# Optimization experiments

Measured on AMD Instinct MI355X. Metric: run time of the kernel, lower is better.

The kernel has to match this reference:

```python
import jax, jax.numpy as jnp
import numpy as np

WINDOW = 3
SEQ_LEN = 41
FEATURE = 128
FILTER_NUM = 128
PAD = WINDOW // 2


def setup_inputs() -> dict:
    key = jax.random.key(0)
    k1, k2 = jax.random.split(key)
    B = 4096
    inputs = jax.random.normal(k1, (B, SEQ_LEN, FEATURE), dtype=jnp.float32)
    # per-position Linear weights: 41 independent [window*feature -> filter_num] layers
    fan_in = WINDOW * FEATURE
    W = jax.random.normal(k2, (SEQ_LEN, fan_in, FILTER_NUM), dtype=jnp.float32) / np.sqrt(fan_in)
    b = jnp.zeros((SEQ_LEN, FILTER_NUM), dtype=jnp.float32)
    return {"inputs": inputs, "W": W, "b": b}


def reference(inputs, W, b):
    # inputs: [B, S, F]; pad sequence dim by PAD zeros on each side
    xpad = jnp.pad(inputs, ((0, 0), (PAD, PAD), (0, 0)))  # [B, S+2*PAD, F]
    # gather windows: idx[s, w] = s + w -> [B, S, WINDOW, F]
    idx = jnp.arange(SEQ_LEN)[:, None] + jnp.arange(WINDOW)[None, :]
    xw = xpad[:, idx, :]
    B = inputs.shape[0]
    xw = xw.reshape(B, SEQ_LEN, WINDOW * FEATURE)  # [B, S, W*F]
    # per-position linear (locally-connected): one batched GEMM over positions
    out = jnp.einsum('bsd,sdf->bsf', xw, W) + b[None, :, :]
    # ReLU; Dropout(0.5) is identity in eval mode
    return jax.nn.relu(out)
```

## Files before the change

kernel.cpp:

```cpp
#include <hip/hip_runtime.h>

#define SEQ 41
#define FEAT 128
#define KDIM 384
#define ROWLEN (SEQ * FEAT)
#define BM 128

typedef float floatx4 __attribute__((ext_vector_type(4)));
typedef __bf16 bf16x8 __attribute__((ext_vector_type(8)));
typedef unsigned short ushortx4 __attribute__((ext_vector_type(4)));
typedef unsigned short ushortx8 __attribute__((ext_vector_type(8)));

__device__ __forceinline__ unsigned short f2bf(float f) {
    unsigned int u = __builtin_bit_cast(unsigned int, f);
    return (unsigned short)((u + 0x7fffu + ((u >> 16) & 1u)) >> 16);
}

#define DMA16(g, l)                                                          \
    __builtin_amdgcn_global_load_lds(                                        \
        (const __attribute__((address_space(1))) void*)(g),                  \
        (__attribute__((address_space(3))) void*)(l), 16, 0, 0)

__global__ __launch_bounds__(256) void wt2_kernel(const float* __restrict__ W,
                                                  unsigned short* __restrict__ Wt2) {
    int t = blockIdx.x * 256 + threadIdx.x;
    int s = t / 6144, g = t % 6144;
    int lane = g & 63, nt = (g >> 6) & 7, ks = (g >> 9) & 1, slab = g >> 10;
    int n  = nt * 16 + (lane & 15);
    int k0 = slab * 64 + ks * 32 + (lane >> 4) * 8;
    const float* Ws = W + (size_t)s * KDIM * FEAT;
    ushortx8 v;
#pragma unroll
    for (int j = 0; j < 8; j++) v[j] = f2bf(Ws[(size_t)(k0 + j) * FEAT + n]);
    *reinterpret_cast<ushortx8*>(Wt2 + (size_t)t * 8) = v;
}

template <int USE_WT>
__global__ __launch_bounds__(256, 2) void gemm_kernel(const float* __restrict__ X,
                                                      const void* __restrict__ Wsrc,
                                                      const float* __restrict__ bias,
                                                      float* __restrict__ out) {
    __shared__ unsigned short Afrag[2][2][8][512];
    __shared__ unsigned short Bfrag[2][2][8][512];

    const int tid  = threadIdx.x;
    const int lane = tid & 63;
    const int wv   = tid >> 6;
    const int s    = blockIdx.y;
    const int m0   = blockIdx.x * BM;

    const int klo = (s == 0) ? 2 : 0;
    const int khi = (s == SEQ - 1) ? 4 : 6;
    const int nk  = khi - klo;
    const int obase = (s - 1) * FEAT;

    const int colq = lane & 15, quad = lane >> 4;
    const int wr = wv >> 1, wc = wv & 1;

    const int ar = tid >> 3;
    const int ag = tid & 7;
    const int aq = ag >> 1, ahalf = ag & 1;

    const unsigned short* Wt2 = (const unsigned short*)Wsrc;
    const float* Wf = (const float*)Wsrc;

    floatx4 acc[4][4];
#pragma unroll
    for (int i = 0; i < 4; i++)
#pragma unroll
        for (int j = 0; j < 4; j++) acc[i][j] = (floatx4){0.f, 0.f, 0.f, 0.f};

    floatx4 a0[4], a1[4];

    auto stageA_load = [&](int kki) {
#pragma unroll
        for (int p = 0; p < 4; p++) {
            const float* base = X + (size_t)(m0 + p * 32 + ar) * ROWLEN
                                  + obase + kki * 64 + ag * 4;
            a0[p] = *reinterpret_cast<const floatx4*>(base);
            a1[p] = *reinterpret_cast<const floatx4*>(base + 32);
        }
    };
    auto stageA_write = [&](int buf) {
#pragma unroll
        for (int p = 0; p < 4; p++) {
            int r  = p * 32 + ar;
            int mt = r >> 4;
            int sl = ((r & 15) + 16 * aq) * 8 + ahalf * 4;
            ushortx4 w0, w1;
#pragma unroll
            for (int e = 0; e < 4; e++) { w0[e] = f2bf(a0[p][e]); w1[e] = f2bf(a1[p][e]); }
            *reinterpret_cast<ushortx4*>(&Afrag[buf][0][mt][sl]) = w0;
            *reinterpret_cast<ushortx4*>(&Afrag[buf][1][mt][sl]) = w1;
        }
    };
    auto stageB = [&](int buf, int kki) {
        if (USE_WT) {
            const unsigned short* src = Wt2 + (size_t)(s * 6 + kki) * 8192;
#pragma unroll
            for (int j = 0; j < 4; j++) {
                int fid = wv * 4 + j;
                const unsigned short* g = src + fid * 512 + lane * 8;
                DMA16(g, &Bfrag[buf][fid >> 3][fid & 7][0]);
            }
        } else {
#pragma unroll
            for (int p = 0; p < 4; p++) {
                int g2 = p * 256 + tid;
                int ln = g2 & 63, nt = (g2 >> 6) & 7, ks = (g2 >> 9) & 1;
                int n = nt * 16 + (ln & 15);
                int k = kki * 64 + ks * 32 + (ln >> 4) * 8;
                ushortx8 v;
#pragma unroll
                for (int j = 0; j < 8; j++)
                    v[j] = f2bf(Wf[((size_t)s * KDIM + k + j) * FEAT + n]);
                *reinterpret_cast<ushortx8*>(&Bfrag[buf][ks][nt][ln * 8]) = v;
            }
        }
    };
    auto compute = [&](int buf) {
#pragma unroll
        for (int ks = 0; ks < 2; ks++) {
            bf16x8 af[4], bf[4];
#pragma unroll
            for (int i = 0; i < 4; i++)
                af[i] = *reinterpret_cast<const bf16x8*>(&Afrag[buf][ks][wr * 4 + i][lane * 8]);
#pragma unroll
            for (int i = 0; i < 4; i++)
                bf[i] = *reinterpret_cast<const bf16x8*>(&Bfrag[buf][ks][wc * 4 + i][lane * 8]);
#pragma unroll
            for (int mi = 0; mi < 4; mi++)
#pragma unroll
                for (int ni = 0; ni < 4; ni++)
                    acc[mi][ni] = __builtin_amdgcn_mfma_f32_16x16x32_bf16(
                        af[mi], bf[ni], acc[mi][ni], 0, 0, 0);
        }
    };

    stageA_load(klo);
    stageB(0, klo);
    stageA_write(0);

    for (int i = 0; i < nk; i++) {
        __syncthreads();
        int cur = i & 1, nxt = cur ^ 1;
        if (i + 1 < nk) {
            stageA_load(klo + i + 1);
            stageB(nxt, klo + i + 1);
        }
        compute(cur);
        if (i + 1 < nk) stageA_write(nxt);
    }

#pragma unroll
    for (int mi = 0; mi < 4; mi++) {
        int m = m0 + (wr * 4 + mi) * 16 + quad * 4;
#pragma unroll
        for (int ni = 0; ni < 4; ni++) {
            int n = (wc * 4 + ni) * 16 + colq;
            float bv = bias[s * FEAT + n];
#pragma unroll
            for (int r = 0; r < 4; r++) {
                float v = acc[mi][ni][r] + bv;
                v = v > 0.f ? v : 0.f;
                out[((size_t)(m + r) * SEQ + s) * FEAT + n] = v;
            }
        }
    }
}

extern "C" void kernel_launch(void* const* d_in, const int* in_sizes, int n_in,
                              void* d_out, int out_size, void* d_ws, size_t ws_size,
                              hipStream_t stream) {
    const float* X    = (const float*)d_in[0];
    const float* W    = (const float*)d_in[1];
    const float* bias = (const float*)d_in[2];
    float* out = (float*)d_out;

    const int B = in_sizes[0] / ROWLEN;
    dim3 grid(B / BM, SEQ);

    const size_t wt_bytes = (size_t)SEQ * 6 * 8192 * sizeof(unsigned short);
    if (ws_size >= wt_bytes) {
        unsigned short* Wt2 = (unsigned short*)d_ws;
        wt2_kernel<<<(SEQ * 6144) / 256, 256, 0, stream>>>(W, Wt2);
        gemm_kernel<1><<<grid, 256, 0, stream>>>(X, (const void*)Wt2, bias, out);
    } else {
        gemm_kernel<0><<<grid, 256, 0, stream>>>(X, (const void*)W, bias, out);
    }
}
```

Before: 184.0 us.

## Drop LDS staging; load MFMA fragments directly from global per wave

```diff
diff --git a/kernel.cpp b/kernel.cpp
--- a/kernel.cpp
+++ b/kernel.cpp
@@ -8,7 +8,6 @@
 
 typedef float floatx4 __attribute__((ext_vector_type(4)));
 typedef __bf16 bf16x8 __attribute__((ext_vector_type(8)));
-typedef unsigned short ushortx4 __attribute__((ext_vector_type(4)));
 typedef unsigned short ushortx8 __attribute__((ext_vector_type(8)));
 
 __device__ __forceinline__ unsigned short f2bf(float f) {
@@ -16,10 +15,12 @@
     return (unsigned short)((u + 0x7fffu + ((u >> 16) & 1u)) >> 16);
 }
 
-#define DMA16(g, l)                                                          \
-    __builtin_amdgcn_global_load_lds(                                        \
-        (const __attribute__((address_space(1))) void*)(g),                  \
-        (__attribute__((address_space(3))) void*)(l), 16, 0, 0)
+__device__ __forceinline__ bf16x8 pack8(floatx4 lo, floatx4 hi) {
+    bf16x8 r;
+#pragma unroll
+    for (int j = 0; j < 4; j++) { r[j] = (__bf16)lo[j]; r[4 + j] = (__bf16)hi[j]; }
+    return r;
+}
 
 __global__ __launch_bounds__(256) void wt2_kernel(const float* __restrict__ W,
                                                   unsigned short* __restrict__ Wt2) {
@@ -36,134 +37,96 @@
 }
 
 template <int USE_WT>
-__global__ __launch_bounds__(256, 2) void gemm_kernel(const float* __restrict__ X,
+__global__ __launch_bounds__(256, 3) void gemm_kernel(const float* __restrict__ X,
                                                       const void* __restrict__ Wsrc,
                                                       const float* __restrict__ bias,
                                                       float* __restrict__ out) {
-    __shared__ unsigned short Afrag[2][2][8][512];
-    __shared__ unsigned short Bfrag[2][2][8][512];
-
     const int tid  = threadIdx.x;
     const int lane = tid & 63;
     const int wv   = tid >> 6;
     const int s    = blockIdx.y;
-    const int m0   = blockIdx.x * BM;
+    const int m0   = blockIdx.x * BM + wv * 32;
 
     const int klo = (s == 0) ? 2 : 0;
     const int khi = (s == SEQ - 1) ? 4 : 6;
-    const int nk  = khi - klo;
-    const int obase = (s - 1) * FEAT;
+    const int nst = (khi - klo) * 2;
 
     const int colq = lane & 15, quad = lane >> 4;
-    const int wr = wv >> 1, wc = wv & 1;
 
-    const int ar = tid >> 3;
-    const int ag = tid & 7;
-    const int aq = ag >> 1, ahalf = ag & 1;
+    const int koff = (s - 1) * FEAT + klo * 64 + quad * 8;
+    const float* aptr0 = X + (size_t)(m0 + colq) * ROWLEN + koff;
+    const float* aptr1 = aptr0 + (size_t)16 * ROWLEN;
 
     const unsigned short* Wt2 = (const unsigned short*)Wsrc;
     const float* Wf = (const float*)Wsrc;
+    const unsigned short* bptr = Wt2 + ((size_t)s * 6 + klo) * 8192 + lane * 8;
 
-    floatx4 acc[4][4];
+    floatx4 acc[2][8];
 #pragma unroll
-    for (int i = 0; i < 4; i++)
+    for (int mi = 0; mi < 2; mi++)
 #pragma unroll
-        for (int j = 0; j < 4; j++) acc[i][j] = (floatx4){0.f, 0.f, 0.f, 0.f};
+        for (int ni = 0; ni < 8; ni++) acc[mi][ni] = (floatx4){0.f, 0.f, 0.f, 0.f};
 
-    floatx4 a0[4], a1[4];
+    floatx4 aL0[2], aH0[2], aL1[2], aH1[2];
 
-    auto stageA_load = [&](int kki) {
+    auto loadA = [&](floatx4 (&L)[2], floatx4 (&H)[2], int ksi) {
+        const float* p0 = aptr0 + ksi * 32;
+        const float* p1 = aptr1 + ksi * 32;
+        L[0] = *reinterpret_cast<const floatx4*>(p0);
+        H[0] = *reinterpret_cast<const floatx4*>(p0 + 4);
+        L[1] = *reinterpret_cast<const floatx4*>(p1);
+        H[1] = *reinterpret_cast<const floatx4*>(p1 + 4);
+    };
+
+    auto step = [&](floatx4 (&L)[2], floatx4 (&H)[2], int ksi) {
+        bf16x8 bfr[8];
+        if (USE_WT) {
+            const unsigned short* bp = bptr + (size_t)ksi * 4096;
 #pragma unroll
-        for (int p = 0; p < 4; p++) {
-            const float* base = X + (size_t)(m0 + p * 32 + ar) * ROWLEN
-                                  + obase + kki * 64 + ag * 4;
-            a0[p] = *reinterpret_cast<const floatx4*>(base);
-            a1[p] = *reinterpret_cast<const floatx4*>(base + 32);
-        }
-    };
-    auto stageA_write = [&](int buf) {
+            for (int ni = 0; ni < 8; ni++)
+                bfr[ni] = *reinterpret_cast<const bf16x8*>(bp + ni * 512);
+        } else {
+            int kk = klo * 64 + ksi * 32 + quad * 8;
 #pragma unroll
-        for (int p = 0; p < 4; p++) {
-            int r  = p * 32 + ar;
-            int mt = r >> 4;
-            int sl = ((r & 15) + 16 * aq) * 8 + ahalf * 4;
-            ushortx4 w0, w1;
-#pragma unroll
-            for (int e = 0; e < 4; e++) { w0[e] = f2bf(a0[p][e]); w1[e] = f2bf(a1[p][e]); }
-            *reinterpret_cast<ushortx4*>(&Afrag[buf][0][mt][sl]) = w0;
-            *reinterpret_cast<ushortx4*>(&Afrag[buf][1][mt][sl]) = w1;
-        }
-    };
-    auto stageB = [&](int buf, int kki) {
-        if (USE_WT) {
-            const unsigned short* src = Wt2 + (size_t)(s * 6 + kki) * 8192;
-#pragma unroll
-            for (int j = 0; j < 4; j++) {
-                int fid = wv * 4 + j;
-                const unsigned short* g = src + fid * 512 + lane * 8;
-                DMA16(g, &Bfrag[buf][fid >> 3][fid & 7][0]);
-            }
-        } else {
-#pragma unroll
-            for (int p = 0; p < 4; p++) {
-                int g2 = p * 256 + tid;
-                int ln = g2 & 63, nt = (g2 >> 6) & 7, ks = (g2 >> 9) & 1;
-                int n = nt * 16 + (ln & 15);
-                int k = kki * 64 + ks * 32 + (ln >> 4) * 8;
+            for (int ni = 0; ni < 8; ni++) {
                 ushortx8 v;
 #pragma unroll
                 for (int j = 0; j < 8; j++)
-                    v[j] = f2bf(Wf[((size_t)s * KDIM + k + j) * FEAT + n]);
-                *reinterpret_cast<ushortx8*>(&Bfrag[buf][ks][nt][ln * 8]) = v;
+                    v[j] = f2bf(Wf[((size_t)s * KDIM + kk + j) * FEAT + ni * 16 + colq]);
+                bfr[ni] = __builtin_bit_cast(bf16x8, v);
             }
         }
-    };
-    auto compute = [&](int buf) {
+        bf16x8 af0 = pack8(L[0], H[0]);
+        bf16x8 af1 = pack8(L[1], H[1]);
+        __builtin_amdgcn_s_setprio(1);
 #pragma unroll
-        for (int ks = 0; ks < 2; ks++) {
-            bf16x8 af[4], bf[4];
-#pragma unroll
-            for (int i = 0; i < 4; i++)
-                af[i] = *reinterpret_cast<const bf16x8*>(&Afrag[buf][ks][wr * 4 + i][lane * 8]);
-#pragma unroll
-            for (int i = 0; i < 4; i++)
-                bf[i] = *reinterpret_cast<const bf16x8*>(&Bfrag[buf][ks][wc * 4 + i][lane * 8]);
-#pragma unroll
-            for (int mi = 0; mi < 4; mi++)
-#pragma unroll
-                for (int ni = 0; ni < 4; ni++)
-                    acc[mi][ni] = __builtin_amdgcn_mfma_f32_16x16x32_bf16(
-                        af[mi], bf[ni], acc[mi][ni], 0, 0, 0);
+        for (int ni = 0; ni < 8; ni++) {
+            acc[0][ni] = __builtin_amdgcn_mfma_f32_16x16x32_bf16(af0, bfr[ni], acc[0][ni], 0, 0, 0);
+            acc[1][ni] = __builtin_amdgcn_mfma_f32_16x16x32_bf16(af1, bfr[ni], acc[1][ni], 0, 0, 0);
         }
+        __builtin_amdgcn_s_setprio(0);
     };
 
-    stageA_load(klo);
-    stageB(0, klo);
-    stageA_write(0);
-
-    for (int i = 0; i < nk; i++) {
-        __syncthreads();
-        int cur = i & 1, nxt = cur ^ 1;
-        if (i + 1 < nk) {
-            stageA_load(klo + i + 1);
-            stageB(nxt, klo + i + 1);
-        }
-        compute(cur);
-        if (i + 1 < nk) stageA_write(nxt);
+    loadA(aL0, aH0, 0);
+    for (int ksi = 0; ksi < nst; ksi += 2) {
+        loadA(aL1, aH1, ksi + 1);
+        step(aL0, aH0, ksi);
+        if (ksi + 2 < nst) loadA(aL0, aH0, ksi + 2);
+        step(aL1, aH1, ksi + 1);
     }
 
 #pragma unroll
-    for (int mi = 0; mi < 4; mi++) {
-        int m = m0 + (wr * 4 + mi) * 16 + quad * 4;
+    for (int ni = 0; ni < 8; ni++) {
+        int n = ni * 16 + colq;
+        float bv = bias[s * FEAT + n];
 #pragma unroll
-        for (int ni = 0; ni < 4; ni++) {
-            int n = (wc * 4 + ni) * 16 + colq;
-            float bv = bias[s * FEAT + n];
+        for (int mi = 0; mi < 2; mi++) {
+            size_t base = ((size_t)(m0 + mi * 16 + quad * 4) * SEQ + s) * FEAT + n;
 #pragma unroll
             for (int r = 0; r < 4; r++) {
                 float v = acc[mi][ni][r] + bv;
                 v = v > 0.f ? v : 0.f;
-                out[((size_t)(m + r) * SEQ + s) * FEAT + n] = v;
+                out[base + (size_t)r * (SEQ * FEAT)] = v;
             }
         }
     }
```

Measured after the change: 202.3 us. 9.9% more time.
